# Optimization experiments

Hardware: AMD Instinct MI355X
Metric: run time of the kernel (lower is better)

## Reference

```python
import jax, jax.numpy as jnp
import numpy as np

T, H, I = 4096, 4096, 11008  # tokens, hidden_size, intermediate_size
QMAX = 127.0


def setup_inputs() -> dict:
    key = jax.random.key(0)
    k0, k1, k2, k3, k4 = jax.random.split(key, 5)
    x = jax.random.normal(k0, (T, H), dtype=jnp.float32)
    # int8 weights stored as float32 integer values in [-127, 127]
    wq_gate_up = jnp.round(jnp.clip(jax.random.normal(k1, (2 * I, H), dtype=jnp.float32) * 30.0, -QMAX, QMAX))
    s_gate_up = jax.random.uniform(k2, (2 * I,), dtype=jnp.float32, minval=5e-4, maxval=2e-3)
    wq_down = jnp.round(jnp.clip(jax.random.normal(k3, (H, I), dtype=jnp.float32) * 30.0, -QMAX, QMAX))
    s_down = jax.random.uniform(k4, (H,), dtype=jnp.float32, minval=5e-4, maxval=2e-3)
    return {"x": x, "wq_gate_up": wq_gate_up, "s_gate_up": s_gate_up,
            "wq_down": wq_down, "s_down": s_down}


def reference(x, wq_gate_up, s_gate_up, wq_down, s_down):
    # --- quantize activations (per-tensor dynamic int8) ---
    x_scale = jnp.max(jnp.abs(x)) / QMAX
    qx = jnp.clip(jnp.round(x / x_scale), -QMAX, QMAX)  # integer-valued f32 (simulated int8)

    # --- gate_up_proj: int8 GEMM (int32 accumulate simulated in f32) ---
    acc = qx @ wq_gate_up.T                             # [T, 2I]
    gate_up = acc * (x_scale * s_gate_up)               # dequant: per-tensor act * per-channel weight scale

    # --- DequantSiluAndMulQuant: silu(gate) * up, then dynamic requant ---
    gate, up = jnp.split(gate_up, 2, axis=-1)           # [T, I] each
    h = jax.nn.silu(gate) * up
    h_scale = jnp.max(jnp.abs(h)) / QMAX
    qh = jnp.clip(jnp.round(h / h_scale), -QMAX, QMAX)

    # --- down_proj: int8 GEMM + dequant ---
    out = (qh @ wq_down.T) * (h_scale * s_down)         # [T, H]
    return out, h_scale
```

## Files before the change

### kernel.cpp

```cpp
#include <hip/hip_runtime.h>

#define T_DIM 4096
#define K1    4096
#define I_DIM 11008
#define QMAXF 127.0f

typedef int v4i  __attribute__((ext_vector_type(4)));


__device__ __forceinline__ void gload16(const void* g, void* l) {
  __builtin_amdgcn_global_load_lds((__attribute__((address_space(1))) unsigned int*)(g),
                                   (__attribute__((address_space(3))) unsigned int*)(l),
                                   16, 0, 0);
}

__device__ __forceinline__ int packq(float a, float b, float c, float d) {
  return ((int)a & 255) | (((int)b & 255) << 8) | (((int)c & 255) << 16) | (((int)d & 255) << 24);
}

#define MFMA(A, B, C) __builtin_amdgcn_mfma_i32_16x16x64_i8(A, B, C, 0, 0, 0)


__global__ void absmax_x_kernel(const float4* __restrict__ x4, unsigned* __restrict__ maxbits, int n4) {
  int tid = blockIdx.x * blockDim.x + threadIdx.x;
  int stride = gridDim.x * blockDim.x;
  float m = 0.f;
  for (int i = tid; i < n4; i += stride) {
    float4 v = x4[i];
    m = fmaxf(m, fmaxf(fmaxf(fabsf(v.x), fabsf(v.y)), fmaxf(fabsf(v.z), fabsf(v.w))));
  }
  #pragma unroll
  for (int off = 32; off; off >>= 1) m = fmaxf(m, __shfl_xor(m, off));
  if ((threadIdx.x & 63) == 0) atomicMax(maxbits, __float_as_uint(m));
}


__global__ void quant_x_kernel(const float4* __restrict__ x4, v4i* __restrict__ q4,
                               const unsigned* __restrict__ scal) {
  const float sx = __uint_as_float(scal[0]) * (1.0f / QMAXF);
  const long i = (long)blockIdx.x * blockDim.x + threadIdx.x;
  v4i o;
  #pragma unroll
  for (int j = 0; j < 4; ++j) {
    float4 v = x4[i * 4 + j];
    float a = fminf(fmaxf(rintf(v.x / sx), -QMAXF), QMAXF);
    float b = fminf(fmaxf(rintf(v.y / sx), -QMAXF), QMAXF);
    float c = fminf(fmaxf(rintf(v.z / sx), -QMAXF), QMAXF);
    float d = fminf(fmaxf(rintf(v.w / sx), -QMAXF), QMAXF);
    o[j] = packq(a, b, c, d);
  }
  q4[i] = o;
}


__global__ void conv_w_kernel(const float4* __restrict__ w4, v4i* __restrict__ q4) {
  const long i = (long)blockIdx.x * blockDim.x + threadIdx.x;
  v4i o;
  #pragma unroll
  for (int j = 0; j < 4; ++j) {
    float4 v = w4[i * 4 + j];
    o[j] = packq(rintf(v.x), rintf(v.y), rintf(v.z), rintf(v.w));
  }
  q4[i] = o;
}


#define STG_A(PTR, SB) { gload16((PTR), &L[SB][lA]); gload16((PTR) + 32, &L[SB][lA + 8192]); }
#define STG_B(PTR, SB) { gload16((PTR), &L[SB][lB]); gload16((PTR) + 32, &L[SB][lB + 8192]); }

#define PH0(CB, SB, APTR, DOST)                                              \
  {                                                                          \
    a0 = *(const v4i*)&L[CB][aoff];                                          \
    a1 = *(const v4i*)&L[CB][aoff + 256];                                    \
    a2 = *(const v4i*)&L[CB][aoff + 512];                                    \
    a3 = *(const v4i*)&L[CB][aoff + 768];                                    \
    b0 = *(const v4i*)&L[CB][boff];                                          \
    b1 = *(const v4i*)&L[CB][boff + 256];                                    \
    b2 = *(const v4i*)&L[CB][boff + 512];                                    \
    b3 = *(const v4i*)&L[CB][boff + 768];                                    \
    if (DOST) STG_A(APTR, SB);                                               \
    __builtin_amdgcn_s_barrier();                                            \
    asm volatile("s_waitcnt lgkmcnt(0)" ::: "memory");                       \
    __builtin_amdgcn_sched_barrier(0);                                       \
    __builtin_amdgcn_s_setprio(1);                                           \
    acc[0][0]=MFMA(a0,b0,acc[0][0]); acc[0][1]=MFMA(a0,b1,acc[0][1]);        \
    acc[0][2]=MFMA(a0,b2,acc[0][2]); acc[0][3]=MFMA(a0,b3,acc[0][3]);        \
    acc[1][0]=MFMA(a1,b0,acc[1][0]); acc[1][1]=MFMA(a1,b1,acc[1][1]);        \
    acc[1][2]=MFMA(a1,b2,acc[1][2]); acc[1][3]=MFMA(a1,b3,acc[1][3]);        \
    acc[2][0]=MFMA(a2,b0,acc[2][0]); acc[2][1]=MFMA(a2,b1,acc[2][1]);        \
    acc[2][2]=MFMA(a2,b2,acc[2][2]); acc[2][3]=MFMA(a2,b3,acc[2][3]);        \
    acc[3][0]=MFMA(a3,b0,acc[3][0]); acc[3][1]=MFMA(a3,b1,acc[3][1]);        \
    acc[3][2]=MFMA(a3,b2,acc[3][2]); acc[3][3]=MFMA(a3,b3,acc[3][3]);        \
    __builtin_amdgcn_s_setprio(0);                                           \
    __builtin_amdgcn_s_barrier();                                            \
    asm volatile("" ::: "memory");                                           \
  }

#define PH1(CB, SB, BPTR, DOST, VM)                                          \
  {                                                                          \
    a0 = *(const v4i*)&L[CB][aoff + 1024];                                   \
    a1 = *(const v4i*)&L[CB][aoff + 1280];                                   \
    a2 = *(const v4i*)&L[CB][aoff + 1536];                                   \
    a3 = *(const v4i*)&L[CB][aoff + 1792];                                   \
    if (DOST) STG_B(BPTR, SB);                                               \
    __builtin_amdgcn_s_barrier();                                            \
    asm volatile("s_waitcnt lgkmcnt(0)" ::: "memory");                       \
    __builtin_amdgcn_sched_barrier(0);                                       \
    __builtin_amdgcn_s_setprio(1);                                           \
    acc[4][0]=MFMA(a0,b0,acc[4][0]); acc[4][1]=MFMA(a0,b1,acc[4][1]);        \
    acc[4][2]=MFMA(a0,b2,acc[4][2]); acc[4][3]=MFMA(a0,b3,acc[4][3]);        \
    acc[5][0]=MFMA(a1,b0,acc[5][0]); acc[5][1]=MFMA(a1,b1,acc[5][1]);        \
    acc[5][2]=MFMA(a1,b2,acc[5][2]); acc[5][3]=MFMA(a1,b3,acc[5][3]);        \
    acc[6][0]=MFMA(a2,b0,acc[6][0]); acc[6][1]=MFMA(a2,b1,acc[6][1]);        \
    acc[6][2]=MFMA(a2,b2,acc[6][2]); acc[6][3]=MFMA(a2,b3,acc[6][3]);        \
    acc[7][0]=MFMA(a3,b0,acc[7][0]); acc[7][1]=MFMA(a3,b1,acc[7][1]);        \
    acc[7][2]=MFMA(a3,b2,acc[7][2]); acc[7][3]=MFMA(a3,b3,acc[7][3]);        \
    __builtin_amdgcn_s_setprio(0);                                           \
    asm volatile("s_waitcnt vmcnt(" VM ")" ::: "memory");                    \
    __builtin_amdgcn_s_barrier();                                            \
    asm volatile("" ::: "memory");                                           \
  }


__global__ __launch_bounds__(512, 2)
void gemm1_silu_kernel(const signed char* __restrict__ qx,
                       const signed char* __restrict__ w8,
                       const float* __restrict__ sgu,
                       unsigned* __restrict__ scal,
                       float* __restrict__ hbuf)
{
  __shared__ signed char L[4][32768];

  const int tid  = threadIdx.x;
  const int lane = tid & 63;
  const int wid  = tid >> 6;
  const int wr   = wid >> 2;
  const int wc   = wid & 3;
  const int ln15 = lane & 15;
  const int kq   = lane >> 4;

  const int lin = blockIdx.x;
  const int sw  = (lin & 7) * 172 + (lin >> 3);
  const int brow = (sw & 15) * 256;
  const int bcol = (sw >> 4) * 128;

  const int sro = tid & 255, skq = tid >> 8;
  const signed char* gA = qx + (size_t)(brow + sro) * K1 + skq * 16;
  const int grp = sro >> 6, w = sro & 63;
  const int gcolw = bcol + grp * 32 + (w & 31);
  const size_t srcrow = (w < 32) ? (size_t)gcolw : (size_t)(I_DIM + gcolw);
  const signed char* gB = w8 + srcrow * K1 + skq * 16;
  const int lA = tid * 16;
  const int lB = 16384 + tid * 16;

  const int aoff = kq * 4096 + (wr * 128 + ln15) * 16;
  const int boff = 16384 + kq * 4096 + (wc * 64 + ln15) * 16;

  v4i acc[8][4];
  #pragma unroll
  for (int m = 0; m < 8; ++m)
    #pragma unroll
    for (int n = 0; n < 4; ++n) acc[m][n] = v4i{0, 0, 0, 0};
  v4i a0, a1, a2, a3, b0, b1, b2, b3;

  STG_A(gA, 0); STG_B(gB, 0);
  STG_A(gA + 64, 1); STG_B(gB + 64, 1);
  asm volatile("s_waitcnt vmcnt(4)" ::: "memory");
  __builtin_amdgcn_s_barrier();
  asm volatile("" ::: "memory");

  const signed char* gAp = gA;
  const signed char* gBp = gB;
  for (int p = 0; p < 15; ++p) {
    PH0(0, 2, gAp + 128, 1) PH1(0, 2, gBp + 128, 1, "4")
    PH0(1, 3, gAp + 192, 1) PH1(1, 3, gBp + 192, 1, "4")
    PH0(2, 0, gAp + 256, 1) PH1(2, 0, gBp + 256, 1, "4")
    PH0(3, 1, gAp + 320, 1) PH1(3, 1, gBp + 320, 1, "4")
    gAp += 256; gBp += 256;
  }
  PH0(0, 2, gAp + 128, 1) PH1(0, 2, gBp + 128, 1, "4")
  PH0(1, 3, gAp + 192, 1) PH1(1, 3, gBp + 192, 1, "4")
  PH0(2, 0, gAp,       0) PH1(2, 0, gBp,       0, "0")
  PH0(3, 1, gAp,       0) PH1(3, 1, gBp,       0, "0")

  const float xsc = __uint_as_float(scal[0]) * (1.0f / QMAXF);
  float hmax = 0.f;
  #pragma unroll
  for (int m = 0; m < 8; ++m) {
    const int row0 = brow + wr * 128 + m * 16 + kq * 4;
    #pragma unroll
    for (int n = 0; n < 2; ++n) {
      const int col = bcol + wc * 32 + n * 16 + ln15;
      const float sg = sgu[col] * xsc;
      const float su = sgu[I_DIM + col] * xsc;
      #pragma unroll
      for (int q = 0; q < 4; ++q) {
        float g = (float)acc[m][n][q] * sg;
        float u = (float)acc[m][n + 2][q] * su;
        float hv = (g / (1.f + expf(-g))) * u;
        hmax = fmaxf(hmax, fabsf(hv));
        hbuf[(size_t)(row0 + q) * I_DIM + col] = hv;
      }
    }
  }
  #pragma unroll
  for (int off = 32; off; off >>= 1) hmax = fmaxf(hmax, __shfl_xor(hmax, off));
  if (lane == 0) atomicMax(scal + 1, __float_as_uint(hmax));
}


__global__ void quant_h_kernel(const float4* __restrict__ h4, v4i* __restrict__ q4,
                               const unsigned* __restrict__ scal) {
  const float hs = __uint_as_float(scal[1]) * (1.0f / QMAXF);
  const long i = (long)blockIdx.x * blockDim.x + threadIdx.x;
  v4i o;
  #pragma unroll
  for (int j = 0; j < 4; ++j) {
    float4 v = h4[i * 4 + j];
    float a = fminf(fmaxf(rintf(v.x / hs), -QMAXF), QMAXF);
    float b = fminf(fmaxf(rintf(v.y / hs), -QMAXF), QMAXF);
    float c = fminf(fmaxf(rintf(v.z / hs), -QMAXF), QMAXF);
    float d = fminf(fmaxf(rintf(v.w / hs), -QMAXF), QMAXF);
    o[j] = packq(a, b, c, d);
  }
  q4[i] = o;
}

__global__ void hscale_out_kernel(const unsigned* __restrict__ scal, float* __restrict__ dst) {
  dst[0] = __uint_as_float(scal[1]) * (1.0f / QMAXF);
}


__global__ __launch_bounds__(512, 2)
void gemm2_kernel(const signed char* __restrict__ qh,
                  const signed char* __restrict__ w8,
                  const float* __restrict__ sdn,
                  const unsigned* __restrict__ scal,
                  float* __restrict__ out)
{
  __shared__ signed char L[4][32768];

  const int tid  = threadIdx.x;
  const int lane = tid & 63;
  const int wid  = tid >> 6;
  const int wr   = wid >> 2;
  const int wc   = wid & 3;
  const int ln15 = lane & 15;
  const int kq   = lane >> 4;

  const int lin = blockIdx.x;
  const int sw  = (lin & 7) * 32 + (lin >> 3);
  const int brow = (sw & 15) * 256;
  const int bcol = (sw >> 4) * 256;

  const int sro = tid & 255, skq = tid >> 8;
  const signed char* gA = qh + (size_t)(brow + sro) * I_DIM + skq * 16;
  const signed char* gB = w8 + (size_t)(bcol + sro) * I_DIM + skq * 16;
  const int lA = tid * 16;
  const int lB = 16384 + tid * 16;

  const int aoff = kq * 4096 + (wr * 128 + ln15) * 16;
  const int boff = 16384 + kq * 4096 + (wc * 64 + ln15) * 16;

  v4i acc[8][4];
  #pragma unroll
  for (int m = 0; m < 8; ++m)
    #pragma unroll
    for (int n = 0; n < 4; ++n) acc[m][n] = v4i{0, 0, 0, 0};
  v4i a0, a1, a2, a3, b0, b1, b2, b3;

  STG_A(gA, 0); STG_B(gB, 0);
  STG_A(gA + 64, 1); STG_B(gB + 64, 1);
  asm volatile("s_waitcnt vmcnt(4)" ::: "memory");
  __builtin_amdgcn_s_barrier();
  asm volatile("" ::: "memory");

  const signed char* gAp = gA;
  const signed char* gBp = gB;
  for (int p = 0; p < 42; ++p) {
    PH0(0, 2, gAp + 128, 1) PH1(0, 2, gBp + 128, 1, "4")
    PH0(1, 3, gAp + 192, 1) PH1(1, 3, gBp + 192, 1, "4")
    PH0(2, 0, gAp + 256, 1) PH1(2, 0, gBp + 256, 1, "4")
    PH0(3, 1, gAp + 320, 1) PH1(3, 1, gBp + 320, 1, "4")
    gAp += 256; gBp += 256;
  }
  PH0(0, 2, gAp + 128, 1) PH1(0, 2, gBp + 128, 1, "4")
  PH0(1, 3, gAp + 192, 1) PH1(1, 3, gBp + 192, 1, "4")
  PH0(2, 0, gAp,       0) PH1(2, 0, gBp,       0, "0")
  PH0(3, 1, gAp,       0) PH1(3, 1, gBp,       0, "0")

  const float hsc = __uint_as_float(scal[1]) * (1.0f / QMAXF);
  #pragma unroll
  for (int m = 0; m < 8; ++m) {
    const int row0 = brow + wr * 128 + m * 16 + kq * 4;
    #pragma unroll
    for (int n = 0; n < 4; ++n) {
      const int col = bcol + wc * 64 + n * 16 + ln15;
      const float s = sdn[col] * hsc;
      #pragma unroll
      for (int q = 0; q < 4; ++q)
        out[(size_t)(row0 + q) * K1 + col] = (float)acc[m][n][q] * s;
    }
  }
}


extern "C" void kernel_launch(void* const* d_in, const int* in_sizes, int n_in,
                              void* d_out, int out_size, void* d_ws, size_t ws_size,
                              hipStream_t stream) {
  (void)in_sizes; (void)n_in; (void)out_size; (void)ws_size;
  const float* x   = (const float*)d_in[0];
  const float* wgu = (const float*)d_in[1];
  const float* sgu = (const float*)d_in[2];
  const float* wdn = (const float*)d_in[3];
  const float* sdn = (const float*)d_in[4];
  float* out = (float*)d_out;
  char* ws = (char*)d_ws;

  signed char* qx  = (signed char*)(ws + 0LL);
  signed char* w8g = (signed char*)(ws + 16777216LL);
  signed char* w8d = (signed char*)(ws + 106954752LL);
  signed char* qh  = (signed char*)(ws + 152043520LL);
  float*       hb  = (float*)      (ws + 197132288LL);
  unsigned*    scal= (unsigned*)   (ws + 377487360LL);

  hipMemsetAsync(scal, 0, 256, stream);
  absmax_x_kernel<<<2048, 256, 0, stream>>>((const float4*)x, scal, T_DIM * K1 / 4);
  quant_x_kernel<<<4096, 256, 0, stream>>>((const float4*)x, (v4i*)qx, scal);
  conv_w_kernel<<<22016, 256, 0, stream>>>((const float4*)wgu, (v4i*)w8g);
  conv_w_kernel<<<11008, 256, 0, stream>>>((const float4*)wdn, (v4i*)w8d);

  gemm1_silu_kernel<<<1376, 512, 0, stream>>>(qx, w8g, sgu, scal, hb);

  quant_h_kernel<<<11008, 256, 0, stream>>>((const float4*)hb, (v4i*)qh, scal);
  hscale_out_kernel<<<1, 1, 0, stream>>>(scal, out + (size_t)T_DIM * K1);

  gemm2_kernel<<<256, 512, 0, stream>>>(qh, w8d, sdn, scal, out);
}
```

Baseline: 1.187 ms.

## Restructure GEMM mainloop: one barrier per K-tile, wave-specialized staging, staggered halves

Replaces the two-phase loop, which had two or three barriers per K-tile, with a single barrier per tile. Each wave now stages only A (waves 0-3) or only B (waves 4-7), issuing four 16-byte loads. The two wave groups also compute their M halves in opposite order, so LDS reads and MFMA bursts are staggered across waves. The aim is to cut barrier stalls and spread LDS bank pressure, at the cost of holding eight A fragments live (more registers) and a riskier buffer-reuse ordering.

Result: slower. 3.524 ms (+197.0%).

```diff
diff --git a/kernel.cpp b/kernel.cpp
--- a/kernel.cpp
+++ b/kernel.cpp
@@ -65,23 +65,28 @@
 }
 
 
-#define STG_A(PTR, SB) { gload16((PTR), &L[SB][lA]); gload16((PTR) + 32, &L[SB][lA + 8192]); }
-#define STG_B(PTR, SB) { gload16((PTR), &L[SB][lB]); gload16((PTR) + 32, &L[SB][lB + 8192]); }
-
-#define PH0(CB, SB, APTR, DOST)                                              \
-  {                                                                          \
-    a0 = *(const v4i*)&L[CB][aoff];                                          \
-    a1 = *(const v4i*)&L[CB][aoff + 256];                                    \
-    a2 = *(const v4i*)&L[CB][aoff + 512];                                    \
-    a3 = *(const v4i*)&L[CB][aoff + 768];                                    \
-    b0 = *(const v4i*)&L[CB][boff];                                          \
-    b1 = *(const v4i*)&L[CB][boff + 256];                                    \
-    b2 = *(const v4i*)&L[CB][boff + 512];                                    \
-    b3 = *(const v4i*)&L[CB][boff + 768];                                    \
-    if (DOST) STG_A(APTR, SB);                                               \
-    __builtin_amdgcn_s_barrier();                                            \
+#define STG4(P, SB) {                                                        \
+    gload16((P),      &L[SB][ldst]);                                         \
+    gload16((P) + 16, &L[SB][ldst + 4096]);                                  \
+    gload16((P) + 32, &L[SB][ldst + 8192]);                                  \
+    gload16((P) + 48, &L[SB][ldst + 12288]);                                 \
+  }
+
+#define WAITDS                                                               \
     asm volatile("s_waitcnt lgkmcnt(0)" ::: "memory");                       \
-    __builtin_amdgcn_sched_barrier(0);                                       \
+    __builtin_amdgcn_sched_barrier(0);
+
+#define RD_A03(CB)                                                           \
+    a0 = *(const v4i*)&L[CB][aoff];        a1 = *(const v4i*)&L[CB][aoff + 256]; \
+    a2 = *(const v4i*)&L[CB][aoff + 512];  a3 = *(const v4i*)&L[CB][aoff + 768];
+#define RD_A47(CB)                                                           \
+    a4 = *(const v4i*)&L[CB][aoff + 1024]; a5 = *(const v4i*)&L[CB][aoff + 1280]; \
+    a6 = *(const v4i*)&L[CB][aoff + 1536]; a7 = *(const v4i*)&L[CB][aoff + 1792];
+#define RD_B(CB)                                                             \
+    b0 = *(const v4i*)&L[CB][boff];        b1 = *(const v4i*)&L[CB][boff + 256]; \
+    b2 = *(const v4i*)&L[CB][boff + 512];  b3 = *(const v4i*)&L[CB][boff + 768];
+
+#define MM_P0                                                                \
     __builtin_amdgcn_s_setprio(1);                                           \
     acc[0][0]=MFMA(a0,b0,acc[0][0]); acc[0][1]=MFMA(a0,b1,acc[0][1]);        \
     acc[0][2]=MFMA(a0,b2,acc[0][2]); acc[0][3]=MFMA(a0,b3,acc[0][3]);        \
@@ -91,34 +96,39 @@
     acc[2][2]=MFMA(a2,b2,acc[2][2]); acc[2][3]=MFMA(a2,b3,acc[2][3]);        \
     acc[3][0]=MFMA(a3,b0,acc[3][0]); acc[3][1]=MFMA(a3,b1,acc[3][1]);        \
     acc[3][2]=MFMA(a3,b2,acc[3][2]); acc[3][3]=MFMA(a3,b3,acc[3][3]);        \
-    __builtin_amdgcn_s_setprio(0);                                           \
-    __builtin_amdgcn_s_barrier();                                            \
-    asm volatile("" ::: "memory");                                           \
-  }
-
-#define PH1(CB, SB, BPTR, DOST, VM)                                          \
+    __builtin_amdgcn_s_setprio(0);
+
+#define MM_P1                                                                \
+    __builtin_amdgcn_s_setprio(1);                                           \
+    acc[4][0]=MFMA(a4,b0,acc[4][0]); acc[4][1]=MFMA(a4,b1,acc[4][1]);        \
+    acc[4][2]=MFMA(a4,b2,acc[4][2]); acc[4][3]=MFMA(a4,b3,acc[4][3]);        \
+    acc[5][0]=MFMA(a5,b0,acc[5][0]); acc[5][1]=MFMA(a5,b1,acc[5][1]);        \
+    acc[5][2]=MFMA(a5,b2,acc[5][2]); acc[5][3]=MFMA(a5,b3,acc[5][3]);        \
+    acc[6][0]=MFMA(a6,b0,acc[6][0]); acc[6][1]=MFMA(a6,b1,acc[6][1]);        \
+    acc[6][2]=MFMA(a6,b2,acc[6][2]); acc[6][3]=MFMA(a6,b3,acc[6][3]);        \
+    acc[7][0]=MFMA(a7,b0,acc[7][0]); acc[7][1]=MFMA(a7,b1,acc[7][1]);        \
+    acc[7][2]=MFMA(a7,b2,acc[7][2]); acc[7][3]=MFMA(a7,b3,acc[7][3]);        \
+    __builtin_amdgcn_s_setprio(0);
+
+#define TILE(CB, SB, KOFF, DOST, VM)                                         \
   {                                                                          \
-    a0 = *(const v4i*)&L[CB][aoff + 1024];                                   \
-    a1 = *(const v4i*)&L[CB][aoff + 1280];                                   \
-    a2 = *(const v4i*)&L[CB][aoff + 1536];                                   \
-    a3 = *(const v4i*)&L[CB][aoff + 1792];                                   \
-    if (DOST) STG_B(BPTR, SB);                                               \
-    __builtin_amdgcn_s_barrier();                                            \
-    asm volatile("s_waitcnt lgkmcnt(0)" ::: "memory");                       \
-    __builtin_amdgcn_sched_barrier(0);                                       \
-    __builtin_amdgcn_s_setprio(1);                                           \
-    acc[4][0]=MFMA(a0,b0,acc[4][0]); acc[4][1]=MFMA(a0,b1,acc[4][1]);        \
-    acc[4][2]=MFMA(a0,b2,acc[4][2]); acc[4][3]=MFMA(a0,b3,acc[4][3]);        \
-    acc[5][0]=MFMA(a1,b0,acc[5][0]); acc[5][1]=MFMA(a1,b1,acc[5][1]);        \
-    acc[5][2]=MFMA(a1,b2,acc[5][2]); acc[5][3]=MFMA(a1,b3,acc[5][3]);        \
-    acc[6][0]=MFMA(a2,b0,acc[6][0]); acc[6][1]=MFMA(a2,b1,acc[6][1]);        \
-    acc[6][2]=MFMA(a2,b2,acc[6][2]); acc[6][3]=MFMA(a2,b3,acc[6][3]);        \
-    acc[7][0]=MFMA(a3,b0,acc[7][0]); acc[7][1]=MFMA(a3,b1,acc[7][1]);        \
-    acc[7][2]=MFMA(a3,b2,acc[7][2]); acc[7][3]=MFMA(a3,b3,acc[7][3]);        \
-    __builtin_amdgcn_s_setprio(0);                                           \
     asm volatile("s_waitcnt vmcnt(" VM ")" ::: "memory");                    \
     __builtin_amdgcn_s_barrier();                                            \
     asm volatile("" ::: "memory");                                           \
+    v4i a0, a1, a2, a3, a4, a5, a6, a7, b0, b1, b2, b3;                      \
+    if (xgrp) {                                                              \
+      RD_A03(CB) RD_B(CB)                                                    \
+      if (DOST) STG4(gS + (KOFF), SB);                                       \
+      WAITDS MM_P0                                                           \
+      RD_A47(CB)                                                             \
+      WAITDS MM_P1                                                           \
+    } else {                                                                 \
+      RD_A47(CB) RD_B(CB)                                                    \
+      if (DOST) STG4(gS + (KOFF), SB);                                       \
+      WAITDS MM_P1                                                           \
+      RD_A03(CB)                                                             \
+      WAITDS MM_P0                                                           \
+    }                                                                        \
   }
 
 
@@ -138,20 +148,21 @@
   const int wc   = wid & 3;
   const int ln15 = lane & 15;
   const int kq   = lane >> 4;
+  const bool xgrp = (wid < 4);
 
   const int lin = blockIdx.x;
   const int sw  = (lin & 7) * 172 + (lin >> 3);
   const int brow = (sw & 15) * 256;
   const int bcol = (sw >> 4) * 128;
 
-  const int sro = tid & 255, skq = tid >> 8;
-  const signed char* gA = qx + (size_t)(brow + sro) * K1 + skq * 16;
+  const int sro = tid & 255;
+  const signed char* gSA = qx + (size_t)(brow + sro) * K1;
   const int grp = sro >> 6, w = sro & 63;
   const int gcolw = bcol + grp * 32 + (w & 31);
   const size_t srcrow = (w < 32) ? (size_t)gcolw : (size_t)(I_DIM + gcolw);
-  const signed char* gB = w8 + srcrow * K1 + skq * 16;
-  const int lA = tid * 16;
-  const int lB = 16384 + tid * 16;
+  const signed char* gSB = w8 + srcrow * K1;
+  const signed char* gS = xgrp ? gSA : gSB;
+  const int ldst = (xgrp ? 0 : 16384) + sro * 16;
 
   const int aoff = kq * 4096 + (wr * 128 + ln15) * 16;
   const int boff = 16384 + kq * 4096 + (wc * 64 + ln15) * 16;
@@ -161,27 +172,23 @@
   for (int m = 0; m < 8; ++m)
     #pragma unroll
     for (int n = 0; n < 4; ++n) acc[m][n] = v4i{0, 0, 0, 0};
-  v4i a0, a1, a2, a3, b0, b1, b2, b3;
-
-  STG_A(gA, 0); STG_B(gB, 0);
-  STG_A(gA + 64, 1); STG_B(gB + 64, 1);
-  asm volatile("s_waitcnt vmcnt(4)" ::: "memory");
-  __builtin_amdgcn_s_barrier();
-  asm volatile("" ::: "memory");
-
-  const signed char* gAp = gA;
-  const signed char* gBp = gB;
+
+  STG4(gS, 0);
+  STG4(gS + 64, 1);
+
+  const signed char* gSp = gS;
   for (int p = 0; p < 15; ++p) {
-    PH0(0, 2, gAp + 128, 1) PH1(0, 2, gBp + 128, 1, "4")
-    PH0(1, 3, gAp + 192, 1) PH1(1, 3, gBp + 192, 1, "4")
-    PH0(2, 0, gAp + 256, 1) PH1(2, 0, gBp + 256, 1, "4")
-    PH0(3, 1, gAp + 320, 1) PH1(3, 1, gBp + 320, 1, "4")
-    gAp += 256; gBp += 256;
-  }
-  PH0(0, 2, gAp + 128, 1) PH1(0, 2, gBp + 128, 1, "4")
-  PH0(1, 3, gAp + 192, 1) PH1(1, 3, gBp + 192, 1, "4")
-  PH0(2, 0, gAp,       0) PH1(2, 0, gBp,       0, "0")
-  PH0(3, 1, gAp,       0) PH1(3, 1, gBp,       0, "0")
+    TILE(0, 2, 128, 1, "4")
+    TILE(1, 3, 192, 1, "4")
+    TILE(2, 0, 256, 1, "4")
+    TILE(3, 1, 320, 1, "4")
+    gS += 256;
+  }
+  TILE(0, 2, 128, 1, "4")
+  TILE(1, 3, 192, 1, "4")
+  TILE(2, 0, 0,   0, "4")
+  TILE(3, 1, 0,   0, "0")
+  gS = gSp;
 
   const float xsc = __uint_as_float(scal[0]) * (1.0f / QMAXF);
   float hmax = 0.f;
@@ -247,17 +254,18 @@
   const int wc   = wid & 3;
   const int ln15 = lane & 15;
   const int kq   = lane >> 4;
+  const bool xgrp = (wid < 4);
 
   const int lin = blockIdx.x;
   const int sw  = (lin & 7) * 32 + (lin >> 3);
   const int brow = (sw & 15) * 256;
   const int bcol = (sw >> 4) * 256;
 
-  const int sro = tid & 255, skq = tid >> 8;
-  const signed char* gA = qh + (size_t)(brow + sro) * I_DIM + skq * 16;
-  const signed char* gB = w8 + (size_t)(bcol + sro) * I_DIM + skq * 16;
-  const int lA = tid * 16;
-  const int lB = 16384 + tid * 16;
+  const int sro = tid & 255;
+  const signed char* gSA = qh + (size_t)(brow + sro) * I_DIM;
+  const signed char* gSB = w8 + (size_t)(bcol + sro) * I_DIM;
+  const signed char* gS = xgrp ? gSA : gSB;
+  const int ldst = (xgrp ? 0 : 16384) + sro * 16;
 
   const int aoff = kq * 4096 + (wr * 128 + ln15) * 16;
   const int boff = 16384 + kq * 4096 + (wc * 64 + ln15) * 16;
@@ -267,27 +275,21 @@
   for (int m = 0; m < 8; ++m)
     #pragma unroll
     for (int n = 0; n < 4; ++n) acc[m][n] = v4i{0, 0, 0, 0};
-  v4i a0, a1, a2, a3, b0, b1, b2, b3;
-
-  STG_A(gA, 0); STG_B(gB, 0);
-  STG_A(gA + 64, 1); STG_B(gB + 64, 1);
-  asm volatile("s_waitcnt vmcnt(4)" ::: "memory");
-  __builtin_amdgcn_s_barrier();
-  asm volatile("" ::: "memory");
-
-  const signed char* gAp = gA;
-  const signed char* gBp = gB;
+
+  STG4(gS, 0);
+  STG4(gS + 64, 1);
+
   for (int p = 0; p < 42; ++p) {
-    PH0(0, 2, gAp + 128, 1) PH1(0, 2, gBp + 128, 1, "4")
-    PH0(1, 3, gAp + 192, 1) PH1(1, 3, gBp + 192, 1, "4")
-    PH0(2, 0, gAp + 256, 1) PH1(2, 0, gBp + 256, 1, "4")
-    PH0(3, 1, gAp + 320, 1) PH1(3, 1, gBp + 320, 1, "4")
-    gAp += 256; gBp += 256;
-  }
-  PH0(0, 2, gAp + 128, 1) PH1(0, 2, gBp + 128, 1, "4")
-  PH0(1, 3, gAp + 192, 1) PH1(1, 3, gBp + 192, 1, "4")
-  PH0(2, 0, gAp,       0) PH1(2, 0, gBp,       0, "0")
-  PH0(3, 1, gAp,       0) PH1(3, 1, gBp,       0, "0")
+    TILE(0, 2, 128, 1, "4")
+    TILE(1, 3, 192, 1, "4")
+    TILE(2, 0, 256, 1, "4")
+    TILE(3, 1, 320, 1, "4")
+    gS += 256;
+  }
+  TILE(0, 2, 128, 1, "4")
+  TILE(1, 3, 192, 1, "4")
+  TILE(2, 0, 0,   0, "4")
+  TILE(3, 1, 0,   0, "0")
 
   const float hsc = __uint_as_float(scal[1]) * (1.0f / QMAXF);
   #pragma unroll
```
